# Kernel tuning notes

Hardware: AMD Instinct MI355X
Metric: run time of the kernel (lower is better)

The kernel has to match this reference:

```python
import jax, jax.numpy as jnp
import numpy as np

B, S, D, M = 4, 1024, 128, 20000
THRESH = 0.1          # memory.query_with_indices threshold
CW_MIN = 0.01         # compound_weight > 0.01 gate
TI_MIN = 0.01         # total_influence > 0.01 gate
NORM_EPS = 1e-6       # norm_sq > 1e-6 gate
INF_EPS = 1e-5        # division epsilon


def setup_inputs() -> dict:
    key = jax.random.key(0)
    ks = jax.random.split(key, 4)
    sd = 1.0 / np.sqrt(D)
    return {
        "input_tensor": jax.random.normal(ks[0], (B, S, D), dtype=jnp.float32),
        "mem": jax.random.normal(ks[1], (M, D), dtype=jnp.float32),
        "W1": jax.random.normal(ks[2], (D, D), dtype=jnp.float32) * sd,
        "b1": jnp.zeros((D,), dtype=jnp.float32),
        "ln_g": jnp.ones((D,), dtype=jnp.float32),
        "ln_b": jnp.zeros((D,), dtype=jnp.float32),
        "W2": jax.random.normal(ks[3], (D, D), dtype=jnp.float32) * sd,
        "b2": jnp.zeros((D,), dtype=jnp.float32),
    }


def reference(input_tensor, mem, W1, b1, ln_g, ln_b, W2, b2):
    x = input_tensor  # [B,S,D]
    # fusion_net: Linear -> LayerNorm -> ReLU
    h = jnp.einsum("bsd,ed->bse", x, W1) + b1
    mu = h.mean(-1, keepdims=True)
    var = h.var(-1, keepdims=True)
    h = (h - mu) * jax.lax.rsqrt(var + 1e-5) * ln_g + ln_b
    feats = jax.nn.relu(h)
    raw = jnp.einsum("bsd,ed->bse", feats, W2) + b2  # [B,S,D]

    # GraphMemory query: cosine similarity, keep entries with sim > THRESH
    xn = x * jax.lax.rsqrt(jnp.sum(x * x, -1, keepdims=True) + 1e-12)
    mn = mem * jax.lax.rsqrt(jnp.sum(mem * mem, -1, keepdims=True) + 1e-12)
    sim = jnp.einsum("bsd,md->bsm", xn, mn)              # [B,S,M]
    w = jnp.where(sim > THRESH, sim, 0.0)                # per-token weights

    # compound_weight per batch & memory slot (sum over seq positions)
    cw = w.sum(axis=1)                                   # [B,M]
    norm_sq = jnp.sum(mem * mem, -1)                     # [M]
    active = (cw > CW_MIN) & (norm_sq > NORM_EPS)        # [B,M]
    eff = jnp.where(active, cw, 0.0)                     # effective weights

    # projection of each target vec onto each memory vec
    safe_ns = jnp.where(norm_sq > NORM_EPS, norm_sq, 1.0)
    coef = jnp.einsum("bsd,md->bsm", raw, mem) / safe_ns # [B,S,M]
    correction = jnp.einsum("bsm,bm,md->bsd", coef, eff, mem)  # [B,S,D]

    ti = eff.sum(-1)                                     # [B] total_influence
    corr = correction / (ti + INF_EPS)[:, None, None]
    final = jnp.where((ti > TI_MIN)[:, None, None], raw + 0.5 * corr, raw)
    return final
```

## Files before the change

### kernel.cpp

```cpp
#include <hip/hip_runtime.h>

#define DD 128
#define SS 1024
#define BB 4
#define M_TOT 20000
#define M_PAD 20480
#define GM_NCH 64
#define GM_CH 320
#define FMLP_BLOCKS 128
#define PREP_BLOCKS 320

typedef __bf16 bf16x8 __attribute__((ext_vector_type(8)));
typedef unsigned short u16x8 __attribute__((ext_vector_type(8)));
typedef float f32x16 __attribute__((ext_vector_type(16)));

union BF8 { bf16x8 b; u16x8 u; };

__device__ __forceinline__ unsigned short f2bf(float f) {
    unsigned int u = __float_as_uint(f);
    u += 0x7FFFu + ((u >> 16) & 1u);
    return (unsigned short)(u >> 16);
}
__device__ __forceinline__ float bf2f(unsigned short h) {
    return __uint_as_float(((unsigned int)h) << 16);
}

__global__ __launch_bounds__(256) void k_front(
    const float* __restrict__ x, const float* __restrict__ W1,
    const float* __restrict__ b1, const float* __restrict__ ln_g,
    const float* __restrict__ ln_b, const float* __restrict__ W2,
    const float* __restrict__ b2, const float* __restrict__ mem,
    unsigned short* __restrict__ xnb, float* __restrict__ raw,
    unsigned short* __restrict__ mnb, unsigned short* __restrict__ mnT,
    float* __restrict__ norm_sq, float* __restrict__ ti,
    float* __restrict__ cw) {
    __shared__ __align__(16) char smem_raw[64 * 136 * 2];
    const int tid = threadIdx.x;
    const int bid = blockIdx.x;

    if (bid < FMLP_BLOCKS) {
        unsigned short* featsL = (unsigned short*)smem_raw;
        float* redp = (float*)(smem_raw + 8704);
        float2* stats = (float2*)(smem_raw + 8704 + 1024);
        const int lane = tid & 63, wv = tid >> 6;
        const int col = lane & 31, hi = lane >> 5;
        const int t0 = bid * 32;
        const int ct = wv;

        bf16x8 Af[8];
        float sq = 0.f;
        const float* xrow = x + (size_t)(t0 + col) * DD + hi * 8;
        #pragma unroll
        for (int kk = 0; kk < 8; ++kk) {
            float4 p = *(const float4*)(xrow + kk * 16);
            float4 q = *(const float4*)(xrow + kk * 16 + 4);
            BF8 t;
            t.u[0] = f2bf(p.x); t.u[1] = f2bf(p.y); t.u[2] = f2bf(p.z); t.u[3] = f2bf(p.w);
            t.u[4] = f2bf(q.x); t.u[5] = f2bf(q.y); t.u[6] = f2bf(q.z); t.u[7] = f2bf(q.w);
            Af[kk] = t.b;
            sq += p.x * p.x + p.y * p.y + p.z * p.z + p.w * p.w;
            sq += q.x * q.x + q.y * q.y + q.z * q.z + q.w * q.w;
        }
        sq += __shfl_xor(sq, 32);
        float xrs = rsqrtf(sq + 1e-12f);
        if (wv == 0) {
            unsigned short* xo = xnb + (size_t)(t0 + col) * DD + hi * 8;
            #pragma unroll
            for (int kk = 0; kk < 8; ++kk) {
                BF8 t; t.b = Af[kk];
                u16x8 o;
                #pragma unroll
                for (int j = 0; j < 8; ++j) o[j] = f2bf(bf2f(t.u[j]) * xrs);
                *(u16x8*)(xo + kk * 16) = o;
            }
        }

        f32x16 acc;
        {
            float bv = b1[ct * 32 + col];
            #pragma unroll
            for (int r = 0; r < 16; ++r) acc[r] = bv;
        }
        const float* w1row = W1 + (size_t)(ct * 32 + col) * DD + hi * 8;
        #pragma unroll
        for (int kk = 0; kk < 8; ++kk) {
            float4 p = *(const float4*)(w1row + kk * 16);
            float4 q = *(const float4*)(w1row + kk * 16 + 4);
            BF8 t;
            t.u[0] = f2bf(p.x); t.u[1] = f2bf(p.y); t.u[2] = f2bf(p.z); t.u[3] = f2bf(p.w);
            t.u[4] = f2bf(q.x); t.u[5] = f2bf(q.y); t.u[6] = f2bf(q.z); t.u[7] = f2bf(q.w);
            acc = __builtin_amdgcn_mfma_f32_32x32x16_bf16(Af[kk], t.b, acc, 0, 0, 0);
        }

        float rs_[16], rq_[16];
        #pragma unroll
        for (int r = 0; r < 16; ++r) { float v = acc[r]; rs_[r] = v; rq_[r] = v * v; }
        #pragma unroll
        for (int off = 1; off < 32; off <<= 1) {
            #pragma unroll
            for (int r = 0; r < 16; ++r) {
                rs_[r] += __shfl_xor(rs_[r], off);
                rq_[r] += __shfl_xor(rq_[r], off);
            }
        }
        if (col == 0) {
            #pragma unroll
            for (int r = 0; r < 16; ++r) {
                int row = (r & 3) + 8 * (r >> 2) + 4 * hi;
                redp[(wv * 32 + row) * 2 + 0] = rs_[r];
                redp[(wv * 32 + row) * 2 + 1] = rq_[r];
            }
        }
        __syncthreads();
        if (tid < 32) {
            float S = redp[(0 * 32 + tid) * 2] + redp[(1 * 32 + tid) * 2] +
                      redp[(2 * 32 + tid) * 2] + redp[(3 * 32 + tid) * 2];
            float Q = redp[(0 * 32 + tid) * 2 + 1] + redp[(1 * 32 + tid) * 2 + 1] +
                      redp[(2 * 32 + tid) * 2 + 1] + redp[(3 * 32 + tid) * 2 + 1];
            float mu = S * (1.f / 128.f);
            float rstd = rsqrtf(Q * (1.f / 128.f) - mu * mu + 1e-5f);
            stats[tid] = make_float2(mu, rstd);
        }
        __syncthreads();

        {
            float gv = ln_g[ct * 32 + col], bv = ln_b[ct * 32 + col];
            #pragma unroll
            for (int r = 0; r < 16; ++r) {
                int row = (r & 3) + 8 * (r >> 2) + 4 * hi;
                float2 st = stats[row];
                float v = fmaxf((acc[r] - st.x) * st.y * gv + bv, 0.f);
                featsL[row * 136 + ct * 32 + col] = f2bf(v);
            }
        }
        __syncthreads();

        f32x16 a2;
        {
            float bv = b2[ct * 32 + col];
            #pragma unroll
            for (int r = 0; r < 16; ++r) a2[r] = bv;
        }
        const float* w2row = W2 + (size_t)(ct * 32 + col) * DD + hi * 8;
        #pragma unroll
        for (int kk = 0; kk < 8; ++kk) {
            bf16x8 Aq = *(const bf16x8*)&featsL[(lane & 31) * 136 + hi * 8 + kk * 16];
            float4 p = *(const float4*)(w2row + kk * 16);
            float4 q = *(const float4*)(w2row + kk * 16 + 4);
            BF8 t;
            t.u[0] = f2bf(p.x); t.u[1] = f2bf(p.y); t.u[2] = f2bf(p.z); t.u[3] = f2bf(p.w);
            t.u[4] = f2bf(q.x); t.u[5] = f2bf(q.y); t.u[6] = f2bf(q.z); t.u[7] = f2bf(q.w);
            a2 = __builtin_amdgcn_mfma_f32_32x32x16_bf16(Aq, t.b, a2, 0, 0, 0);
        }
        #pragma unroll
        for (int r = 0; r < 16; ++r) {
            int row = (r & 3) + 8 * (r >> 2) + 4 * hi;
            raw[(size_t)(t0 + row) * DD + ct * 32 + col] = a2[r];
        }
    } else {
        unsigned short* RM = (unsigned short*)smem_raw;
        const int pb = bid - FMLP_BLOCKS;
        const int m0 = pb * 64;
        cw[pb * 256 + tid] = 0.0f;
        if (pb == 0 && tid < BB) ti[tid] = 0.0f;

        const int r = tid >> 2, seg = tid & 3;
        const int m = m0 + r;
        const bool ok = m < M_TOT;
        float4 v[8];
        const float4* src = (const float4*)mem + (size_t)m * 32 + seg * 8;
        #pragma unroll
        for (int i = 0; i < 8; ++i)
            v[i] = ok ? src[i] : make_float4(0.f, 0.f, 0.f, 0.f);
        float ss = 0.f;
        #pragma unroll
        for (int i = 0; i < 8; ++i)
            ss += v[i].x * v[i].x + v[i].y * v[i].y + v[i].z * v[i].z + v[i].w * v[i].w;
        ss += __shfl_xor(ss, 1);
        ss += __shfl_xor(ss, 2);
        float rs = rsqrtf(ss + 1e-12f);
        if (seg == 0) norm_sq[m] = ss;

        #pragma unroll
        for (int i = 0; i < 4; ++i) {
            float4 a = v[2 * i], bq = v[2 * i + 1];
            u16x8 o;
            o[0] = f2bf(a.x * rs); o[1] = f2bf(a.y * rs);
            o[2] = f2bf(a.z * rs); o[3] = f2bf(a.w * rs);
            o[4] = f2bf(bq.x * rs); o[5] = f2bf(bq.y * rs);
            o[6] = f2bf(bq.z * rs); o[7] = f2bf(bq.w * rs);
            *(u16x8*)(mnb + (size_t)m * DD + seg * 32 + i * 8) = o;
            *(u16x8*)(RM + r * 136 + seg * 32 + i * 8) = o;
        }
        __syncthreads();
        const int d = tid >> 1, half = tid & 1;
        unsigned short* dst = mnT + (size_t)d * M_PAD + m0 + half * 32;
        #pragma unroll
        for (int q = 0; q < 4; ++q) {
            u16x8 o;
            #pragma unroll
            for (int j = 0; j < 8; ++j)
                o[j] = RM[(half * 32 + q * 8 + j) * 136 + d];
            *(u16x8*)(dst + q * 8) = o;
        }
    }
}

__global__ __launch_bounds__(256, 3) void k_cw(
    const unsigned short* __restrict__ xnb, const unsigned short* __restrict__ mnb,
    float* __restrict__ cw) {
    __shared__ unsigned short As[4][32 * 128];
    const int tid = threadIdx.x, lane = tid & 63, wv = tid >> 6;
    const int c = lane & 31, h = lane >> 5;
    const int b = blockIdx.z;
    const int mw = blockIdx.x * 256 + wv * 64;
    const int s_base = blockIdx.y * 256;

    const int srow = tid >> 4, sk16 = tid & 15;
    const int soff = srow * 128 + ((sk16 * 8) ^ ((srow & 15) << 3));
    const int srow1 = srow + 16;
    const int soff1 = srow1 * 128 + ((sk16 * 8) ^ ((srow1 & 15) << 3));
    const unsigned short* xbase = xnb + ((size_t)b * SS + s_base) * DD;

    bf16x8 Bf[2][8];
    #pragma unroll
    for (int ct = 0; ct < 2; ++ct)
        #pragma unroll
        for (int kk = 0; kk < 8; ++kk)
            Bf[ct][kk] = *(const bf16x8*)(mnb + (size_t)(mw + ct * 32 + c) * DD +
                                          kk * 16 + h * 8);

    {
        u16x8 a0 = *(const u16x8*)(xbase + (size_t)srow * DD + sk16 * 8);
        u16x8 a1 = *(const u16x8*)(xbase + (size_t)srow1 * DD + sk16 * 8);
        const unsigned short* n1 = xbase + (size_t)32 * DD;
        u16x8 b0 = *(const u16x8*)(n1 + (size_t)srow * DD + sk16 * 8);
        u16x8 b1 = *(const u16x8*)(n1 + (size_t)srow1 * DD + sk16 * 8);
        *(u16x8*)&As[0][soff] = a0; *(u16x8*)&As[0][soff1] = a1;
        *(u16x8*)&As[1][soff] = b0; *(u16x8*)&As[1][soff1] = b1;
    }

    float cw0 = 0.f, cw1 = 0.f;
    #pragma unroll 1
    for (int p = 0; p < 4; ++p) {
        __syncthreads();
        u16x8 w0, w1, w2, w3;
        if (p < 3) {
            const unsigned short* n0 = xbase + (size_t)(2 * p + 2) * 32 * DD;
            const unsigned short* n1 = xbase + (size_t)(2 * p + 3) * 32 * DD;
            w0 = *(const u16x8*)(n0 + (size_t)srow * DD + sk16 * 8);
            w1 = *(const u16x8*)(n0 + (size_t)srow1 * DD + sk16 * 8);
            w2 = *(const u16x8*)(n1 + (size_t)srow * DD + sk16 * 8);
            w3 = *(const u16x8*)(n1 + (size_t)srow1 * DD + sk16 * 8);
        }
        {
            f32x16 p0, p1;
            #pragma unroll
            for (int r = 0; r < 16; ++r) { p0[r] = 0.f; p1[r] = 0.f; }
            const unsigned short* Ab = As[(2 * p) & 3];
            __builtin_amdgcn_s_setprio(1);
            #pragma unroll
            for (int kk = 0; kk < 8; ++kk) {
                bf16x8 Afr = *(const bf16x8*)&Ab[c * 128 + ((kk * 16 + h * 8) ^ ((c & 15) << 3))];
                p0 = __builtin_amdgcn_mfma_f32_32x32x16_bf16(Afr, Bf[0][kk], p0, 0, 0, 0);
                p1 = __builtin_amdgcn_mfma_f32_32x32x16_bf16(Afr, Bf[1][kk], p1, 0, 0, 0);
            }
            __builtin_amdgcn_s_setprio(0);
            #pragma unroll
            for (int r = 0; r < 16; ++r) {
                float a = p0[r], bb = p1[r];
                cw0 += a > 0.1f ? a : 0.f;
                cw1 += bb > 0.1f ? bb : 0.f;
            }
        }
        {
            f32x16 p0, p1;
            #pragma unroll
            for (int r = 0; r < 16; ++r) { p0[r] = 0.f; p1[r] = 0.f; }
            const unsigned short* Ab = As[(2 * p + 1) & 3];
            __builtin_amdgcn_s_setprio(1);
            #pragma unroll
            for (int kk = 0; kk < 8; ++kk) {
                bf16x8 Afr = *(const bf16x8*)&Ab[c * 128 + ((kk * 16 + h * 8) ^ ((c & 15) << 3))];
                p0 = __builtin_amdgcn_mfma_f32_32x32x16_bf16(Afr, Bf[0][kk], p0, 0, 0, 0);
                p1 = __builtin_amdgcn_mfma_f32_32x32x16_bf16(Afr, Bf[1][kk], p1, 0, 0, 0);
            }
            __builtin_amdgcn_s_setprio(0);
            if (p < 3) {
                unsigned short* An0 = As[(2 * p + 2) & 3];
                unsigned short* An1 = As[(2 * p + 3) & 3];
                *(u16x8*)&An0[soff] = w0; *(u16x8*)&An0[soff1] = w1;
                *(u16x8*)&An1[soff] = w2; *(u16x8*)&An1[soff1] = w3;
            }
            #pragma unroll
            for (int r = 0; r < 16; ++r) {
                float a = p0[r], bb = p1[r];
                cw0 += a > 0.1f ? a : 0.f;
                cw1 += bb > 0.1f ? bb : 0.f;
            }
        }
    }
    cw0 += __shfl_xor(cw0, 32);
    cw1 += __shfl_xor(cw1, 32);
    if (lane < 32) {
        atomicAdd(&cw[(size_t)b * M_PAD + mw + c], cw0);
        atomicAdd(&cw[(size_t)b * M_PAD + mw + 32 + c], cw1);
    }
}

__global__ __launch_bounds__(256) void k_gmatm(
    const unsigned short* __restrict__ mnT, const float* __restrict__ cw,
    const float* __restrict__ norm_sq, float* __restrict__ ti,
    float* __restrict__ pG) {
    __shared__ float effL[GM_CH];
    __shared__ float rb[4];
    const int tid = threadIdx.x, lane = tid & 63, wv = tid >> 6;
    const int c = lane & 31, h = lane >> 5;
    const int half = blockIdx.y;
    const int b = blockIdx.z;
    const int m0 = blockIdx.x * GM_CH;

    float tsum = 0.f;
    #pragma unroll
    for (int idx = tid; idx < GM_CH; idx += 256) {
        int m = m0 + idx;
        float e = 0.f;
        if (m < M_TOT) {
            float cc = cw[(size_t)b * M_PAD + m];
            float ns = norm_sq[m];
            e = (cc > 0.01f && ns > 1e-6f) ? cc : 0.f;
        }
        effL[idx] = e;
        tsum += e;
    }
    #pragma unroll
    for (int off = 1; off < 64; off <<= 1) tsum += __shfl_xor(tsum, off);
    if (lane == 0) rb[wv] = tsum;
    __syncthreads();
    if (half == 0 && tid == 0) atomicAdd(&ti[b], rb[0] + rb[1] + rb[2] + rb[3]);

    const int rbase = half * 64 + (wv >> 1) * 32;
    const int ct0 = (wv & 1) * 2;

    f32x16 a0, a1;
    #pragma unroll
    for (int r = 0; r < 16; ++r) { a0[r] = 0.f; a1[r] = 0.f; }

    const unsigned short* Arow = mnT + (size_t)(rbase + c) * M_PAD;
    const unsigned short* B0r = mnT + (size_t)((ct0 + 0) * 32 + c) * M_PAD;
    const unsigned short* B1r = mnT + (size_t)((ct0 + 1) * 32 + c) * M_PAD;

    #pragma unroll 1
    for (int t = 0; t < GM_CH / 64; ++t) {
        #pragma unroll
        for (int kk = 0; kk < 4; ++kk) {
            const int mo = m0 + t * 64 + kk * 16 + h * 8;
            const int eo = t * 64 + kk * 16 + h * 8;
            u16x8 au = *(const u16x8*)(Arow + mo);
            float4 e0 = *(float4*)&effL[eo];
            float4 e1 = *(float4*)&effL[eo + 4];
            BF8 af;
            af.u[0] = f2bf(bf2f(au[0]) * e0.x);
            af.u[1] = f2bf(bf2f(au[1]) * e0.y);
            af.u[2] = f2bf(bf2f(au[2]) * e0.z);
            af.u[3] = f2bf(bf2f(au[3]) * e0.w);
            af.u[4] = f2bf(bf2f(au[4]) * e1.x);
            af.u[5] = f2bf(bf2f(au[5]) * e1.y);
            af.u[6] = f2bf(bf2f(au[6]) * e1.z);
            af.u[7] = f2bf(bf2f(au[7]) * e1.w);
            bf16x8 B0 = *(const bf16x8*)(B0r + mo);
            bf16x8 B1 = *(const bf16x8*)(B1r + mo);
            a0 = __builtin_amdgcn_mfma_f32_32x32x16_bf16(af.b, B0, a0, 0, 0, 0);
            a1 = __builtin_amdgcn_mfma_f32_32x32x16_bf16(af.b, B1, a1, 0, 0, 0);
        }
    }
    float* o = pG + (size_t)(blockIdx.x * BB + b) * (DD * DD);
    #pragma unroll
    for (int r = 0; r < 16; ++r) {
        int rf = (r & 3) + 8 * (r >> 2) + 4 * h;
        o[(rbase + rf) * DD + (ct0 + 0) * 32 + c] = a0[r];
        o[(rbase + rf) * DD + (ct0 + 1) * 32 + c] = a1[r];
    }
}

__global__ __launch_bounds__(256) void k_gmat2(const float* __restrict__ pG,
                                               unsigned short* __restrict__ Gb) {
    __shared__ float4 redv[256];
    const int tid = threadIdx.x;
    const int b = blockIdx.y;
    const int f4i = blockIdx.x * 64 + (tid & 63);
    const int cg = tid >> 6;
    const float4* pG4 = (const float4*)pG;
    float4 s = make_float4(0.f, 0.f, 0.f, 0.f);
    for (int c = cg; c < GM_NCH; c += 4) {
        float4 p = pG4[(size_t)(c * BB + b) * (DD * DD / 4) + f4i];
        s.x += p.x; s.y += p.y; s.z += p.z; s.w += p.w;
    }
    redv[tid] = s;
    __syncthreads();
    if (tid < 64) {
        float4 r0 = redv[tid], r1 = redv[tid + 64], r2 = redv[tid + 128], r3 = redv[tid + 192];
        ushort4 o;
        o.x = f2bf(r0.x + r1.x + r2.x + r3.x);
        o.y = f2bf(r0.y + r1.y + r2.y + r3.y);
        o.z = f2bf(r0.z + r1.z + r2.z + r3.z);
        o.w = f2bf(r0.w + r1.w + r2.w + r3.w);
        *(ushort4*)&Gb[(size_t)b * (DD * DD) + f4i * 4] = o;
    }
}

__global__ __launch_bounds__(256) void k_final(
    const float* __restrict__ raw, const unsigned short* __restrict__ Gb,
    const float* __restrict__ ti, float* __restrict__ out) {
    const int tid = threadIdx.x, lane = tid & 63, wv = tid >> 6;
    const int col = lane & 31, hi = lane >> 5;
    const int t0 = blockIdx.x * 32;
    const int b = blockIdx.x >> 5;
    const int ct = wv;

    bf16x8 Af[8];
    const float* rrow = raw + (size_t)(t0 + col) * DD + hi * 8;
    #pragma unroll
    for (int kk = 0; kk < 8; ++kk) {
        float4 p = *(const float4*)(rrow + kk * 16);
        float4 q = *(const float4*)(rrow + kk * 16 + 4);
        BF8 t;
        t.u[0] = f2bf(p.x); t.u[1] = f2bf(p.y); t.u[2] = f2bf(p.z); t.u[3] = f2bf(p.w);
        t.u[4] = f2bf(q.x); t.u[5] = f2bf(q.y); t.u[6] = f2bf(q.z); t.u[7] = f2bf(q.w);
        Af[kk] = t.b;
    }
    f32x16 acc;
    #pragma unroll
    for (int r = 0; r < 16; ++r) acc[r] = 0.f;
    const unsigned short* grow = Gb + (size_t)b * DD * DD + (size_t)(ct * 32 + col) * DD + hi * 8;
    #pragma unroll
    for (int kk = 0; kk < 8; ++kk) {
        bf16x8 Bw = *(const bf16x8*)(grow + kk * 16);
        acc = __builtin_amdgcn_mfma_f32_32x32x16_bf16(Af[kk], Bw, acc, 0, 0, 0);
    }
    float tib = ti[b];
    float scale = (tib > 0.01f) ? 0.5f / (tib + 1e-5f) : 0.0f;
    #pragma unroll
    for (int r = 0; r < 16; ++r) {
        int row = (r & 3) + 8 * (r >> 2) + 4 * hi;
        size_t idx = (size_t)(t0 + row) * DD + ct * 32 + col;
        out[idx] = raw[idx] + scale * acc[r];
    }
}

extern "C" void kernel_launch(void* const* d_in, const int* in_sizes, int n_in,
                              void* d_out, int out_size, void* d_ws, size_t ws_size,
                              hipStream_t stream) {
    const float* x   = (const float*)d_in[0];
    const float* mem = (const float*)d_in[1];
    const float* W1  = (const float*)d_in[2];
    const float* b1  = (const float*)d_in[3];
    const float* lg  = (const float*)d_in[4];
    const float* lb  = (const float*)d_in[5];
    const float* W2  = (const float*)d_in[6];
    const float* b2  = (const float*)d_in[7];
    float* out = (float*)d_out;

    float* wsf = (float*)d_ws;
    size_t off = 0;
    unsigned short* mnb = (unsigned short*)(wsf + off); off += (size_t)M_PAD * 64;
    unsigned short* mnT = (unsigned short*)(wsf + off); off += (size_t)M_PAD * 64;
    float* norm_sq = wsf + off;                         off += M_PAD;
    unsigned short* xnb = (unsigned short*)(wsf + off); off += (size_t)BB * SS * 64;
    float* raw = wsf + off;                             off += (size_t)BB * SS * DD;
    float* cw  = wsf + off;                             off += (size_t)BB * M_PAD;
    unsigned short* Gb = (unsigned short*)(wsf + off);  off += (size_t)BB * DD * DD / 2;
    float* ti  = wsf + off;                             off += BB;
    float* pG  = wsf + off;                             off += (size_t)GM_NCH * BB * DD * DD;

    k_front<<<dim3(FMLP_BLOCKS + PREP_BLOCKS), 256, 0, stream>>>(
        x, W1, b1, lg, lb, W2, b2, mem, xnb, raw, mnb, mnT, norm_sq, ti, cw);
    k_cw<<<dim3(M_PAD / 256, 4, BB), 256, 0, stream>>>(xnb, mnb, cw);
    k_gmatm<<<dim3(GM_NCH, 2, BB), 256, 0, stream>>>(mnT, cw, norm_sq, ti, pG);
    k_gmat2<<<dim3(DD * DD / 256, BB), 256, 0, stream>>>(pG, Gb);
    k_final<<<dim3(SS * BB / 32), 256, 0, stream>>>(raw, Gb, ti, out);
}
```

Measured before the change: 78.48 us.

## Replace split-K partial Gram reduction with atomic accumulation and fp16 packed scaling

Removes the separate partial-Gram reduction kernel and its large partial buffer. Each Gram block now computes all 128 columns and atomically adds fp32 results into a G buffer that the front kernel zeroes. The transposed memory copy is stored as fp16, so effective weights scale it with a packed half multiply instead of per-element bf16 round trips, using f16 MFMA. The final kernel converts fp32 G to bf16 on load. This trades one launch and the partial-buffer memory traffic for atomic contention (64 chunks per element) and fp16 range risk for large cw values.

```diff
diff --git a/kernel.cpp b/kernel.cpp
--- a/kernel.cpp
+++ b/kernel.cpp
@@ -11,15 +11,15 @@
 #define PREP_BLOCKS 320
 
 typedef __bf16 bf16x8 __attribute__((ext_vector_type(8)));
+typedef _Float16 f16x8 __attribute__((ext_vector_type(8)));
 typedef unsigned short u16x8 __attribute__((ext_vector_type(8)));
 typedef float f32x16 __attribute__((ext_vector_type(16)));
 
 union BF8 { bf16x8 b; u16x8 u; };
 
 __device__ __forceinline__ unsigned short f2bf(float f) {
-    unsigned int u = __float_as_uint(f);
-    u += 0x7FFFu + ((u >> 16) & 1u);
-    return (unsigned short)(u >> 16);
+    __bf16 h = (__bf16)f;
+    return __builtin_bit_cast(unsigned short, h);
 }
 __device__ __forceinline__ float bf2f(unsigned short h) {
     return __uint_as_float(((unsigned int)h) << 16);
@@ -31,9 +31,9 @@
     const float* __restrict__ ln_b, const float* __restrict__ W2,
     const float* __restrict__ b2, const float* __restrict__ mem,
     unsigned short* __restrict__ xnb, float* __restrict__ raw,
-    unsigned short* __restrict__ mnb, unsigned short* __restrict__ mnT,
+    unsigned short* __restrict__ mnb, _Float16* __restrict__ mnT,
     float* __restrict__ norm_sq, float* __restrict__ ti,
-    float* __restrict__ cw) {
+    float* __restrict__ cw, float* __restrict__ G) {
     __shared__ __align__(16) char smem_raw[64 * 136 * 2];
     const int tid = threadIdx.x;
     const int bid = blockIdx.x;
@@ -162,6 +162,8 @@
         const int pb = bid - FMLP_BLOCKS;
         const int m0 = pb * 64;
         cw[pb * 256 + tid] = 0.0f;
+        if (pb < 64) ((float4*)G)[pb * 256 + tid] =
+            make_float4(0.f, 0.f, 0.f, 0.f);
         if (pb == 0 && tid < BB) ti[tid] = 0.0f;
 
         const int r = tid >> 2, seg = tid & 3;
@@ -194,14 +196,14 @@
         }
         __syncthreads();
         const int d = tid >> 1, half = tid & 1;
-        unsigned short* dst = mnT + (size_t)d * M_PAD + m0 + half * 32;
+        _Float16* dst = mnT + (size_t)d * M_PAD + m0 + half * 32;
         #pragma unroll
         for (int q = 0; q < 4; ++q) {
-            u16x8 o;
+            f16x8 o;
             #pragma unroll
             for (int j = 0; j < 8; ++j)
-                o[j] = RM[(half * 32 + q * 8 + j) * 136 + d];
-            *(u16x8*)(dst + q * 8) = o;
+                o[j] = (_Float16)bf2f(RM[(half * 32 + q * 8 + j) * 136 + d]);
+            *(f16x8*)(dst + q * 8) = o;
         }
     }
 }
@@ -309,15 +311,14 @@
 }
 
 __global__ __launch_bounds__(256) void k_gmatm(
-    const unsigned short* __restrict__ mnT, const float* __restrict__ cw,
+    const _Float16* __restrict__ mnT, const float* __restrict__ cw,
     const float* __restrict__ norm_sq, float* __restrict__ ti,
-    float* __restrict__ pG) {
-    __shared__ float effL[GM_CH];
+    float* __restrict__ G) {
+    __shared__ __align__(16) _Float16 effH[GM_CH];
     __shared__ float rb[4];
     const int tid = threadIdx.x, lane = tid & 63, wv = tid >> 6;
     const int c = lane & 31, h = lane >> 5;
-    const int half = blockIdx.y;
-    const int b = blockIdx.z;
+    const int b = blockIdx.y;
     const int m0 = blockIdx.x * GM_CH;
 
     float tsum = 0.f;
@@ -330,87 +331,56 @@
             float ns = norm_sq[m];
             e = (cc > 0.01f && ns > 1e-6f) ? cc : 0.f;
         }
-        effL[idx] = e;
+        effH[idx] = (_Float16)e;
         tsum += e;
     }
     #pragma unroll
     for (int off = 1; off < 64; off <<= 1) tsum += __shfl_xor(tsum, off);
     if (lane == 0) rb[wv] = tsum;
     __syncthreads();
-    if (half == 0 && tid == 0) atomicAdd(&ti[b], rb[0] + rb[1] + rb[2] + rb[3]);
-
-    const int rbase = half * 64 + (wv >> 1) * 32;
-    const int ct0 = (wv & 1) * 2;
-
-    f32x16 a0, a1;
-    #pragma unroll
-    for (int r = 0; r < 16; ++r) { a0[r] = 0.f; a1[r] = 0.f; }
-
-    const unsigned short* Arow = mnT + (size_t)(rbase + c) * M_PAD;
-    const unsigned short* B0r = mnT + (size_t)((ct0 + 0) * 32 + c) * M_PAD;
-    const unsigned short* B1r = mnT + (size_t)((ct0 + 1) * 32 + c) * M_PAD;
+    if (tid == 0) atomicAdd(&ti[b], rb[0] + rb[1] + rb[2] + rb[3]);
+
+    f32x16 a0, a1, a2, a3;
+    #pragma unroll
+    for (int r = 0; r < 16; ++r) { a0[r] = 0.f; a1[r] = 0.f; a2[r] = 0.f; a3[r] = 0.f; }
+
+    const _Float16* Arow = mnT + (size_t)(wv * 32 + c) * M_PAD + m0;
+    const _Float16* B0r = mnT + (size_t)(0 * 32 + c) * M_PAD + m0;
+    const _Float16* B1r = mnT + (size_t)(1 * 32 + c) * M_PAD + m0;
+    const _Float16* B2r = mnT + (size_t)(2 * 32 + c) * M_PAD + m0;
+    const _Float16* B3r = mnT + (size_t)(3 * 32 + c) * M_PAD + m0;
 
     #pragma unroll 1
     for (int t = 0; t < GM_CH / 64; ++t) {
         #pragma unroll
         for (int kk = 0; kk < 4; ++kk) {
-            const int mo = m0 + t * 64 + kk * 16 + h * 8;
-            const int eo = t * 64 + kk * 16 + h * 8;
-            u16x8 au = *(const u16x8*)(Arow + mo);
-            float4 e0 = *(float4*)&effL[eo];
-            float4 e1 = *(float4*)&effL[eo + 4];
-            BF8 af;
-            af.u[0] = f2bf(bf2f(au[0]) * e0.x);
-            af.u[1] = f2bf(bf2f(au[1]) * e0.y);
-            af.u[2] = f2bf(bf2f(au[2]) * e0.z);
-            af.u[3] = f2bf(bf2f(au[3]) * e0.w);
-            af.u[4] = f2bf(bf2f(au[4]) * e1.x);
-            af.u[5] = f2bf(bf2f(au[5]) * e1.y);
-            af.u[6] = f2bf(bf2f(au[6]) * e1.z);
-            af.u[7] = f2bf(bf2f(au[7]) * e1.w);
-            bf16x8 B0 = *(const bf16x8*)(B0r + mo);
-            bf16x8 B1 = *(const bf16x8*)(B1r + mo);
-            a0 = __builtin_amdgcn_mfma_f32_32x32x16_bf16(af.b, B0, a0, 0, 0, 0);
-            a1 = __builtin_amdgcn_mfma_f32_32x32x16_bf16(af.b, B1, a1, 0, 0, 0);
-        }
-    }
-    float* o = pG + (size_t)(blockIdx.x * BB + b) * (DD * DD);
+            const int mo = t * 64 + kk * 16 + h * 8;
+            f16x8 au = *(const f16x8*)(Arow + mo);
+            f16x8 ef = *(const f16x8*)&effH[mo];
+            f16x8 af = au * ef;
+            f16x8 B0 = *(const f16x8*)(B0r + mo);
+            f16x8 B1 = *(const f16x8*)(B1r + mo);
+            f16x8 B2 = *(const f16x8*)(B2r + mo);
+            f16x8 B3 = *(const f16x8*)(B3r + mo);
+            a0 = __builtin_amdgcn_mfma_f32_32x32x16_f16(af, B0, a0, 0, 0, 0);
+            a1 = __builtin_amdgcn_mfma_f32_32x32x16_f16(af, B1, a1, 0, 0, 0);
+            a2 = __builtin_amdgcn_mfma_f32_32x32x16_f16(af, B2, a2, 0, 0, 0);
+            a3 = __builtin_amdgcn_mfma_f32_32x32x16_f16(af, B3, a3, 0, 0, 0);
+        }
+    }
+    float* Gb = G + (size_t)b * DD * DD;
     #pragma unroll
     for (int r = 0; r < 16; ++r) {
         int rf = (r & 3) + 8 * (r >> 2) + 4 * h;
-        o[(rbase + rf) * DD + (ct0 + 0) * 32 + c] = a0[r];
-        o[(rbase + rf) * DD + (ct0 + 1) * 32 + c] = a1[r];
-    }
-}
-
-__global__ __launch_bounds__(256) void k_gmat2(const float* __restrict__ pG,
-                                               unsigned short* __restrict__ Gb) {
-    __shared__ float4 redv[256];
-    const int tid = threadIdx.x;
-    const int b = blockIdx.y;
-    const int f4i = blockIdx.x * 64 + (tid & 63);
-    const int cg = tid >> 6;
-    const float4* pG4 = (const float4*)pG;
-    float4 s = make_float4(0.f, 0.f, 0.f, 0.f);
-    for (int c = cg; c < GM_NCH; c += 4) {
-        float4 p = pG4[(size_t)(c * BB + b) * (DD * DD / 4) + f4i];
-        s.x += p.x; s.y += p.y; s.z += p.z; s.w += p.w;
-    }
-    redv[tid] = s;
-    __syncthreads();
-    if (tid < 64) {
-        float4 r0 = redv[tid], r1 = redv[tid + 64], r2 = redv[tid + 128], r3 = redv[tid + 192];
-        ushort4 o;
-        o.x = f2bf(r0.x + r1.x + r2.x + r3.x);
-        o.y = f2bf(r0.y + r1.y + r2.y + r3.y);
-        o.z = f2bf(r0.z + r1.z + r2.z + r3.z);
-        o.w = f2bf(r0.w + r1.w + r2.w + r3.w);
-        *(ushort4*)&Gb[(size_t)b * (DD * DD) + f4i * 4] = o;
+        atomicAdd(&Gb[(wv * 32 + rf) * DD + 0 * 32 + c], a0[r]);
+        atomicAdd(&Gb[(wv * 32 + rf) * DD + 1 * 32 + c], a1[r]);
+        atomicAdd(&Gb[(wv * 32 + rf) * DD + 2 * 32 + c], a2[r]);
+        atomicAdd(&Gb[(wv * 32 + rf) * DD + 3 * 32 + c], a3[r]);
     }
 }
 
 __global__ __launch_bounds__(256) void k_final(
-    const float* __restrict__ raw, const unsigned short* __restrict__ Gb,
+    const float* __restrict__ raw, const float* __restrict__ G,
     const float* __restrict__ ti, float* __restrict__ out) {
     const int tid = threadIdx.x, lane = tid & 63, wv = tid >> 6;
     const int col = lane & 31, hi = lane >> 5;
@@ -432,11 +402,15 @@
     f32x16 acc;
     #pragma unroll
     for (int r = 0; r < 16; ++r) acc[r] = 0.f;
-    const unsigned short* grow = Gb + (size_t)b * DD * DD + (size_t)(ct * 32 + col) * DD + hi * 8;
+    const float* grow = G + (size_t)b * DD * DD + (size_t)(ct * 32 + col) * DD + hi * 8;
     #pragma unroll
     for (int kk = 0; kk < 8; ++kk) {
-        bf16x8 Bw = *(const bf16x8*)(grow + kk * 16);
-        acc = __builtin_amdgcn_mfma_f32_32x32x16_bf16(Af[kk], Bw, acc, 0, 0, 0);
+        float4 p = *(const float4*)(grow + kk * 16);
+        float4 q = *(const float4*)(grow + kk * 16 + 4);
+        BF8 t;
+        t.u[0] = f2bf(p.x); t.u[1] = f2bf(p.y); t.u[2] = f2bf(p.z); t.u[3] = f2bf(p.w);
+        t.u[4] = f2bf(q.x); t.u[5] = f2bf(q.y); t.u[6] = f2bf(q.z); t.u[7] = f2bf(q.w);
+        acc = __builtin_amdgcn_mfma_f32_32x32x16_bf16(Af[kk], t.b, acc, 0, 0, 0);
     }
     float tib = ti[b];
     float scale = (tib > 0.01f) ? 0.5f / (tib + 1e-5f) : 0.0f;
@@ -464,19 +438,17 @@
     float* wsf = (float*)d_ws;
     size_t off = 0;
     unsigned short* mnb = (unsigned short*)(wsf + off); off += (size_t)M_PAD * 64;
-    unsigned short* mnT = (unsigned short*)(wsf + off); off += (size_t)M_PAD * 64;
+    _Float16* mnT = (_Float16*)(wsf + off);             off += (size_t)M_PAD * 64;
     float* norm_sq = wsf + off;                         off += M_PAD;
     unsigned short* xnb = (unsigned short*)(wsf + off); off += (size_t)BB * SS * 64;
     float* raw = wsf + off;                             off += (size_t)BB * SS * DD;
     float* cw  = wsf + off;                             off += (size_t)BB * M_PAD;
-    unsigned short* Gb = (unsigned short*)(wsf + off);  off += (size_t)BB * DD * DD / 2;
+    float* G   = wsf + off;                             off += (size_t)BB * DD * DD;
     float* ti  = wsf + off;                             off += BB;
-    float* pG  = wsf + off;                             off += (size_t)GM_NCH * BB * DD * DD;
 
     k_front<<<dim3(FMLP_BLOCKS + PREP_BLOCKS), 256, 0, stream>>>(
-        x, W1, b1, lg, lb, W2, b2, mem, xnb, raw, mnb, mnT, norm_sq, ti, cw);
+        x, W1, b1, lg, lb, W2, b2, mem, xnb, raw, mnb, mnT, norm_sq, ti, cw, G);
     k_cw<<<dim3(M_PAD / 256, 4, BB), 256, 0, stream>>>(xnb, mnb, cw);
-    k_gmatm<<<dim3(GM_NCH, 2, BB), 256, 0, stream>>>(mnT, cw, norm_sq, ti, pG);
-    k_gmat2<<<dim3(DD * DD / 256, BB), 256, 0, stream>>>(pG, Gb);
-    k_final<<<dim3(SS * BB / 32), 256, 0, stream>>>(raw, Gb, ti, out);
-}
+    k_gmatm<<<dim3(GM_NCH, BB), 256, 0, stream>>>(mnT, cw, norm_sq, ti, G);
+    k_final<<<dim3(SS * BB / 32), 256, 0, stream>>>(raw, G, ti, out);
+}
```

Result: slower. 83.96 us (+7.0%).
